# Kernel optimization log

Hardware: AMD Instinct MI355X
Metric: run time of the kernel (lower is better)

## Reference

```python
import jax, jax.numpy as jnp
import numpy as np

TOTAL_LABELS = 81
TOTAL_POS = 128
TOTAL_NEG = 384


def _randomly_select_mask(key, mask, count):
    """Replicates rpn_utils.randomly_select_xyz_mask: keep at most `count`
    randomly-chosen True entries per row (axis=1)."""
    rnd = jax.random.randint(key, mask.shape, 1, count * 10, dtype=jnp.int32)
    scored = mask.astype(jnp.int32) * rnd          # 0 where mask False
    order = jnp.argsort(-scored, axis=1)           # descending sort indices
    rank = jnp.argsort(order, axis=1)              # rank of each position
    return mask & (rank < count)


def setup_inputs() -> dict:
    key = jax.random.key(0)
    k1, k2, k3, k4, k5, k6 = jax.random.split(key, 6)
    B, N, M = 32, 6000, 128
    # Valid normalized boxes (y1,x1,y2,x2): corner + positive extent
    roi_tl = jax.random.uniform(k1, (B, N, 2), minval=0.0, maxval=0.8)
    roi_wh = jax.random.uniform(k2, (B, N, 2), minval=0.01, maxval=0.2)
    roi_bboxes = jnp.concatenate([roi_tl, roi_tl + roi_wh], axis=-1)
    gt_tl = jax.random.uniform(k3, (B, M, 2), minval=0.0, maxval=0.8)
    gt_wh = jax.random.uniform(k4, (B, M, 2), minval=0.05, maxval=0.2)
    gt_boxes = jnp.concatenate([gt_tl, gt_tl + gt_wh], axis=-1)
    gt_labels = jax.random.randint(k5, (B, M), 0, TOTAL_LABELS, dtype=jnp.int32)
    return {"roi_bboxes": roi_bboxes, "gt_boxes": gt_boxes, "gt_labels": gt_labels}


def reference(roi_bboxes, gt_boxes, gt_labels):
    # ---- pairwise IoU (faithful, incl. original gt_area==0 bug) ----
    by1, bx1, by2, bx2 = jnp.split(roi_bboxes, 4, axis=-1)   # each [B,N,1]
    gy1, gx1, gy2, gx2 = jnp.split(gt_boxes, 4, axis=-1)     # each [B,M,1]
    gt_area = jnp.squeeze((gy2 - gy1) * (gx2 - gx2), axis=-1)  # == 0 (original bug)
    bbox_area = jnp.squeeze((by2 - by1) * (bx2 - bx1), axis=-1)
    x_top = jnp.maximum(bx1, jnp.swapaxes(gx1, 1, 2))
    y_top = jnp.maximum(by1, jnp.swapaxes(gy1, 1, 2))
    x_bot = jnp.minimum(bx2, jnp.swapaxes(gx2, 1, 2))
    y_bot = jnp.minimum(by2, jnp.swapaxes(gy2, 1, 2))
    inter = jnp.maximum(x_bot - x_top, 0.0) * jnp.maximum(y_bot - y_top, 0.0)  # [B,N,M]
    union = bbox_area[..., None] + gt_area[:, None, :] - inter
    iou_map = inter / union

    max_idx = jnp.argmax(iou_map, axis=2)   # [B,N]
    merged = jnp.max(iou_map, axis=2)       # [B,N]

    # ---- random positive / negative sampling ----
    skey = jax.random.key(42)
    kp, kn = jax.random.split(skey)
    pos_mask = _randomly_select_mask(kp, merged > 0.5, TOTAL_POS)
    neg_mask = _randomly_select_mask(kn, (merged < 0.5) & (merged > 0.1), TOTAL_NEG)

    # ---- gather matched GT boxes/labels (batch_dims=1 gather) ----
    gt_boxes_map = jax.vmap(lambda g, i: g[i])(gt_boxes, max_idx)     # [B,N,4]
    gt_labels_map = jax.vmap(lambda g, i: g[i])(gt_labels, max_idx)   # [B,N]
    exp_gt = jnp.where(pos_mask[..., None], gt_boxes_map, 0.0)
    pos_lab = jnp.where(pos_mask, gt_labels_map, jnp.int32(-1))
    exp_lab = pos_lab + neg_mask.astype(jnp.int32)  # neg -> 0 (background)

    # ---- bbox delta encoding ----
    bw = roi_bboxes[..., 3] - roi_bboxes[..., 1]
    bh = roi_bboxes[..., 2] - roi_bboxes[..., 0]
    bcx = roi_bboxes[..., 1] + 0.5 * bw
    bcy = roi_bboxes[..., 0] + 0.5 * bh
    gw = exp_gt[..., 3] - exp_gt[..., 1]
    gh = exp_gt[..., 2] - exp_gt[..., 0]
    gcx = exp_gt[..., 1] + 0.5 * gw
    gcy = exp_gt[..., 0] + 0.5 * gh
    bw = jnp.where(bw == 0, 1e-3, bw)
    bh = jnp.where(bh == 0, 1e-3, bh)
    gw_safe = jnp.where(gw == 0, 1.0, gw)  # safe-where: same fwd values, no NaN
    gh_safe = jnp.where(gh == 0, 1.0, gh)
    dx = jnp.where(gw == 0, 0.0, (gcx - bcx) / bw)
    dy = jnp.where(gh == 0, 0.0, (gcy - bcy) / bh)
    dw = jnp.where(gw == 0, 0.0, jnp.log(gw_safe / bw))
    dh = jnp.where(gh == 0, 0.0, jnp.log(gh_safe / bh))
    deltas = jnp.stack([dy, dx, dh, dw], axis=-1)  # [B,N,4]

    # ---- one-hot scatter-multiply ----
    roi_bbox_labels = jax.nn.one_hot(exp_lab, TOTAL_LABELS, dtype=deltas.dtype)  # [B,N,L]; -1 -> all-zero
    roi_bbox_deltas = roi_bbox_labels[..., None] * deltas[:, :, None, :]          # [B,N,L,4]
    return roi_bbox_deltas, roi_bbox_labels
```

## Files before the change

### kernel.cpp

```cpp
#include <hip/hip_runtime.h>
#include <stdint.h>

#define NB 32
#define NN 6000
#define NM 128
#define NL 81
#define NT (NB * NN)
#define SPAN_P 1279u
#define MULT_P 882u
#define SPAN_N 3839u
#define MULT_N 1588u
#define K_POS 128u
#define K_NEG 384u

#define OUT_FLOATS ((size_t)NT * NL * 5)
#define OUT_VEC4 (OUT_FLOATS / 4)

__host__ __device__ __forceinline__ uint32_t rotl32(uint32_t v, uint32_t r) {
  return (v << r) | (v >> (32u - r));
}

__host__ __device__ inline void threefry2x32(uint32_t k0, uint32_t k1,
                                             uint32_t x0, uint32_t x1,
                                             uint32_t& o0, uint32_t& o1) {
  uint32_t kb = k0 ^ k1 ^ 0x1BD11BDAu;
#define TF_ROUND(r) { x0 += x1; x1 = rotl32(x1, r); x1 ^= x0; }
  x0 += k0; x1 += k1;
  TF_ROUND(13u) TF_ROUND(15u) TF_ROUND(26u) TF_ROUND(6u)
  x0 += k1; x1 += kb + 1u;
  TF_ROUND(17u) TF_ROUND(29u) TF_ROUND(16u) TF_ROUND(24u)
  x0 += kb; x1 += k0 + 2u;
  TF_ROUND(13u) TF_ROUND(15u) TF_ROUND(26u) TF_ROUND(6u)
  x0 += k0; x1 += k1 + 3u;
  TF_ROUND(17u) TF_ROUND(29u) TF_ROUND(16u) TF_ROUND(24u)
  x0 += k1; x1 += kb + 4u;
  TF_ROUND(13u) TF_ROUND(15u) TF_ROUND(26u) TF_ROUND(6u)
  x0 += kb; x1 += k0 + 5u;
#undef TF_ROUND
  o0 = x0; o1 = x1;
}

__global__ __launch_bounds__(256) void iou_mask_score(
    const float* __restrict__ roi, const float* __restrict__ gt,
    uint16_t* __restrict__ scp, uint16_t* __restrict__ scn,
    uint8_t* __restrict__ midx, float* __restrict__ out,
    uint32_t k1p0, uint32_t k1p1, uint32_t k2p0, uint32_t k2p1,
    uint32_t k1n0, uint32_t k1n1, uint32_t k2n0, uint32_t k2n1)
{
#pragma clang fp contract(off)
  __shared__ float4 g[NM];
  int b = blockIdx.y;
  if (threadIdx.x < NM)
    g[threadIdx.x] = reinterpret_cast<const float4*>(gt)[b * NM + threadIdx.x];
  __syncthreads();

  {
    float4* o4 = reinterpret_cast<float4*>(out);
    const float4 z = make_float4(0.0f, 0.0f, 0.0f, 0.0f);
    uint32_t gthreads = gridDim.x * gridDim.y * 256u;
    uint32_t i0 = (blockIdx.y * gridDim.x + blockIdx.x) * 256u + threadIdx.x;
    for (uint32_t i = i0; i < (uint32_t)OUT_VEC4; i += gthreads)
      o4[i] = z;
  }

  int n = blockIdx.x * 256 + threadIdx.x;
  if (n >= NN) return;
  size_t t = (size_t)b * NN + n;
  float4 r = reinterpret_cast<const float4*>(roi)[t];
  float by1 = r.x, bx1 = r.y, by2 = r.z, bx2 = r.w;
  float area = (by2 - by1) * (bx2 - bx1);
  float best = -INFINITY; int bi = 0;
  for (int j = 0; j < NM; ++j) {
    float4 q = g[j];
    float xt = fmaxf(bx1, q.y), yt = fmaxf(by1, q.x);
    float xb = fminf(bx2, q.w), yb = fminf(by2, q.z);
    float inter = fmaxf(xb - xt, 0.0f) * fmaxf(yb - yt, 0.0f);
    float uni = area - inter;
    float iou = inter / uni;
    if (iou > best) { best = iou; bi = j; }
  }
  bool pos = best > 0.5f;
  bool neg = (best < 0.5f) && (best > 0.1f);
  uint16_t sp = 0, sn = 0;
  uint32_t a0, a1;
  if (pos) {
    uint32_t h, l;
    threefry2x32(k1p0, k1p1, 0u, (uint32_t)t, a0, a1); h = a0 ^ a1;
    threefry2x32(k2p0, k2p1, 0u, (uint32_t)t, a0, a1); l = a0 ^ a1;
    sp = (uint16_t)(1u + ((h % SPAN_P) * MULT_P + (l % SPAN_P)) % SPAN_P);
  }
  if (neg) {
    uint32_t h, l;
    threefry2x32(k1n0, k1n1, 0u, (uint32_t)t, a0, a1); h = a0 ^ a1;
    threefry2x32(k2n0, k2n1, 0u, (uint32_t)t, a0, a1); l = a0 ^ a1;
    sn = (uint16_t)(1u + ((h % SPAN_N) * MULT_N + (l % SPAN_N)) % SPAN_N);
  }
  scp[t] = sp; scn[t] = sn; midx[t] = (uint8_t)bi;
}

__global__ __launch_bounds__(256) void select_write(
    const uint16_t* __restrict__ scp, const uint16_t* __restrict__ scn,
    const uint8_t* __restrict__ midx,
    const float* __restrict__ roi, const float* __restrict__ gt,
    const int* __restrict__ glab,
    float* __restrict__ out)
{
#pragma clang fp contract(off)
  __shared__ uint32_t hist[3840];
  __shared__ uint32_t csum[256];
  __shared__ uint32_t cpref[256];
  __shared__ int shT;
  __shared__ uint32_t shRem;
  int tid = threadIdx.x;
  int b = blockIdx.x & 31;
  int type = blockIdx.x >> 5;
  const uint16_t* sc = (type ? scn : scp) + (size_t)b * NN;
  const int S = type ? 3840 : 1280;
  const uint32_t K = type ? K_NEG : K_POS;

  for (int s = tid; s < S; s += 256) hist[s] = 0u;
  if (tid == 0) { shT = 0; shRem = 0u; }
  __syncthreads();
  for (int n = tid; n < NN; n += 256) {
    uint32_t s = sc[n];
    if (s) atomicAdd(&hist[s], 1u);
  }
  __syncthreads();
  const int cb = S >> 8;
  int lo = tid * cb, hi = lo + cb;
  uint32_t ms = 0;
  for (int s = lo; s < hi; ++s) ms += hist[s];
  csum[tid] = ms;
  __syncthreads();
  if (tid == 0) {
    uint32_t run = 0;
    for (int c = 255; c >= 0; --c) { cpref[c] = run; run += csum[c]; }
  }
  __syncthreads();
  {
    uint32_t cum = cpref[tid];
    for (int s = hi - 1; s >= lo; --s) {
      uint32_t h = hist[s];
      if (h != 0u && cum < K && cum + h >= K) { shT = s; shRem = K - cum; }
      cum += h;
    }
  }
  __syncthreads();
  const int T = shT;
  const uint32_t rem = shRem;
  const int CH = 24;
  int n0 = tid * CH, n1 = n0 + CH; if (n1 > NN) n1 = NN;
  uint32_t ec = 0;
  if (T > 0) { for (int n = n0; n < n1; ++n) if (sc[n] == (uint16_t)T) ++ec; }
  csum[tid] = ec;
  __syncthreads();
  if (tid == 0) { uint32_t run = 0; for (int c = 0; c < 256; ++c) { cpref[c] = run; run += csum[c]; } }
  __syncthreads();
  uint32_t tr = cpref[tid];
  const size_t labBase = (size_t)NT * NL * 4;
  for (int n = n0; n < n1; ++n) {
    uint32_t s = sc[n];
    if (!s) continue;
    bool keep;
    if ((int)s > T) keep = true;
    else if ((int)s == T) { keep = (tr < rem); ++tr; }
    else keep = false;
    if (!keep) continue;
    size_t t = (size_t)b * NN + n;
    if (type) {
      out[labBase + t * (size_t)NL] = 1.0f;
    } else {
      int mi = midx[t];
      int lab = glab[b * NM + mi];
      float4 r = reinterpret_cast<const float4*>(roi)[t];
      float4 q = reinterpret_cast<const float4*>(gt)[(size_t)b * NM + mi];
      float by1 = r.x, bx1 = r.y, by2 = r.z, bx2 = r.w;
      float gy1 = q.x, gx1 = q.y, gy2 = q.z, gx2 = q.w;
      float bw = bx2 - bx1, bh = by2 - by1;
      float bcx = bx1 + 0.5f * bw, bcy = by1 + 0.5f * bh;
      float gw = gx2 - gx1, gh = gy2 - gy1;
      float gcx = gx1 + 0.5f * gw, gcy = gy1 + 0.5f * gh;
      if (bw == 0.0f) bw = 1e-3f;
      if (bh == 0.0f) bh = 1e-3f;
      float dx = (gw == 0.0f) ? 0.0f : (gcx - bcx) / bw;
      float dy = (gh == 0.0f) ? 0.0f : (gcy - bcy) / bh;
      float dw = (gw == 0.0f) ? 0.0f : logf(gw / bw);
      float dh = (gh == 0.0f) ? 0.0f : logf(gh / bh);
      float4 d; d.x = dy; d.y = dx; d.z = dh; d.w = dw;
      reinterpret_cast<float4*>(out)[t * (size_t)NL + lab] = d;
      out[labBase + t * (size_t)NL + lab] = 1.0f;
    }
  }
}

extern "C" void kernel_launch(void* const* d_in, const int* in_sizes, int n_in,
                              void* d_out, int out_size, void* d_ws, size_t ws_size,
                              hipStream_t stream) {
  (void)in_sizes; (void)n_in; (void)ws_size; (void)out_size;
  const float* roi = (const float*)d_in[0];
  const float* gt  = (const float*)d_in[1];
  const int* glab  = (const int*)d_in[2];
  float* out = (float*)d_out;

  uint16_t* scp = (uint16_t*)d_ws;
  uint16_t* scn = scp + NT;
  uint8_t*  midx = (uint8_t*)(scn + NT);

  uint32_t kp0, kp1, kn0, kn1;
  threefry2x32(0u, 42u, 0u, 0u, kp0, kp1);
  threefry2x32(0u, 42u, 0u, 1u, kn0, kn1);
  uint32_t k1p0, k1p1, k2p0, k2p1, k1n0, k1n1, k2n0, k2n1;
  threefry2x32(kp0, kp1, 0u, 0u, k1p0, k1p1);
  threefry2x32(kp0, kp1, 0u, 1u, k2p0, k2p1);
  threefry2x32(kn0, kn1, 0u, 0u, k1n0, k1n1);
  threefry2x32(kn0, kn1, 0u, 1u, k2n0, k2n1);

  dim3 gridA(24, 32);
  iou_mask_score<<<gridA, 256, 0, stream>>>(roi, gt, scp, scn, midx, out,
      k1p0, k1p1, k2p0, k2p1, k1n0, k1n1, k2n0, k2n1);
  select_write<<<64, 256, 0, stream>>>(scp, scn, midx, roi, gt, glab, out);
}
```

Baseline: 365.8 us.

## Write dense output in one final pass from compact per-ROI label and delta

The output is no longer zeroed and then scatter-patched. The selection kernel now records a compact per-ROI label and delta in workspace, and a new third kernel writes every float4 of the dense one-hot delta and label tensors in one coalesced pass. This removes the zero-fill loop from the IoU kernel and the scattered writes into the large output. The cost is an extra kernel launch, small extra workspace reads, and integer division per output element.

```diff
diff --git a/kernel.cpp b/kernel.cpp
--- a/kernel.cpp
+++ b/kernel.cpp
@@ -13,8 +13,11 @@
 #define K_POS 128u
 #define K_NEG 384u
 
-#define OUT_FLOATS ((size_t)NT * NL * 5)
-#define OUT_VEC4 (OUT_FLOATS / 4)
+#define DELTA_FLOATS ((size_t)NT * NL * 4)
+#define LABEL_FLOATS ((size_t)NT * NL)
+#define DELTA_VEC4 (DELTA_FLOATS / 4)
+#define LABEL_VEC4 (LABEL_FLOATS / 4)
+#define TOTAL_VEC4 (DELTA_VEC4 + LABEL_VEC4)
 
 __host__ __device__ __forceinline__ uint32_t rotl32(uint32_t v, uint32_t r) {
   return (v << r) | (v >> (32u - r));
@@ -43,7 +46,7 @@
 __global__ __launch_bounds__(256) void iou_mask_score(
     const float* __restrict__ roi, const float* __restrict__ gt,
     uint16_t* __restrict__ scp, uint16_t* __restrict__ scn,
-    uint8_t* __restrict__ midx, float* __restrict__ out,
+    uint8_t* __restrict__ midx, int* __restrict__ dlab,
     uint32_t k1p0, uint32_t k1p1, uint32_t k2p0, uint32_t k2p1,
     uint32_t k1n0, uint32_t k1n1, uint32_t k2n0, uint32_t k2n1)
 {
@@ -53,16 +56,6 @@
   if (threadIdx.x < NM)
     g[threadIdx.x] = reinterpret_cast<const float4*>(gt)[b * NM + threadIdx.x];
   __syncthreads();
-
-  {
-    float4* o4 = reinterpret_cast<float4*>(out);
-    const float4 z = make_float4(0.0f, 0.0f, 0.0f, 0.0f);
-    uint32_t gthreads = gridDim.x * gridDim.y * 256u;
-    uint32_t i0 = (blockIdx.y * gridDim.x + blockIdx.x) * 256u + threadIdx.x;
-    for (uint32_t i = i0; i < (uint32_t)OUT_VEC4; i += gthreads)
-      o4[i] = z;
-  }
-
   int n = blockIdx.x * 256 + threadIdx.x;
   if (n >= NN) return;
   size_t t = (size_t)b * NN + n;
@@ -96,14 +89,15 @@
     sn = (uint16_t)(1u + ((h % SPAN_N) * MULT_N + (l % SPAN_N)) % SPAN_N);
   }
   scp[t] = sp; scn[t] = sn; midx[t] = (uint8_t)bi;
-}
-
-__global__ __launch_bounds__(256) void select_write(
+  dlab[t] = -1;
+}
+
+__global__ __launch_bounds__(256) void select_mark(
     const uint16_t* __restrict__ scp, const uint16_t* __restrict__ scn,
     const uint8_t* __restrict__ midx,
     const float* __restrict__ roi, const float* __restrict__ gt,
     const int* __restrict__ glab,
-    float* __restrict__ out)
+    int* __restrict__ dlab, float4* __restrict__ ddelta)
 {
 #pragma clang fp contract(off)
   __shared__ uint32_t hist[3840];
@@ -157,7 +151,6 @@
   if (tid == 0) { uint32_t run = 0; for (int c = 0; c < 256; ++c) { cpref[c] = run; run += csum[c]; } }
   __syncthreads();
   uint32_t tr = cpref[tid];
-  const size_t labBase = (size_t)NT * NL * 4;
   for (int n = n0; n < n1; ++n) {
     uint32_t s = sc[n];
     if (!s) continue;
@@ -168,7 +161,8 @@
     if (!keep) continue;
     size_t t = (size_t)b * NN + n;
     if (type) {
-      out[labBase + t * (size_t)NL] = 1.0f;
+      dlab[t] = 0;
+      ddelta[t] = make_float4(0.0f, 0.0f, 0.0f, 0.0f);
     } else {
       int mi = midx[t];
       int lab = glab[b * NM + mi];
@@ -186,10 +180,48 @@
       float dy = (gh == 0.0f) ? 0.0f : (gcy - bcy) / bh;
       float dw = (gw == 0.0f) ? 0.0f : logf(gw / bw);
       float dh = (gh == 0.0f) ? 0.0f : logf(gh / bh);
-      float4 d; d.x = dy; d.y = dx; d.z = dh; d.w = dw;
-      reinterpret_cast<float4*>(out)[t * (size_t)NL + lab] = d;
-      out[labBase + t * (size_t)NL + lab] = 1.0f;
+      dlab[t] = lab;
+      ddelta[t] = make_float4(dy, dx, dh, dw);
     }
+  }
+}
+
+__global__ __launch_bounds__(256) void write_out(
+    const int* __restrict__ dlab, const float4* __restrict__ ddelta,
+    float4* __restrict__ out4)
+{
+  const float4 z = make_float4(0.0f, 0.0f, 0.0f, 0.0f);
+  uint32_t gsz = gridDim.x * 256u;
+  for (uint32_t i = blockIdx.x * 256u + threadIdx.x; i < (uint32_t)TOTAL_VEC4; i += gsz) {
+    float4 v = z;
+    if (i < (uint32_t)DELTA_VEC4) {
+      uint32_t t = i / (uint32_t)NL;
+      uint32_t s = i - t * (uint32_t)NL;
+      int L = dlab[t];
+      if ((int)s == L) v = ddelta[t];
+    } else {
+      uint32_t f = (i - (uint32_t)DELTA_VEC4) * 4u;
+      uint32_t t = f / (uint32_t)NL;
+      uint32_t s = f - t * (uint32_t)NL;
+      if (s <= (uint32_t)(NL - 4)) {
+        int L = dlab[t];
+        v.x = ((int)s     == L) ? 1.0f : 0.0f;
+        v.y = ((int)s + 1 == L) ? 1.0f : 0.0f;
+        v.z = ((int)s + 2 == L) ? 1.0f : 0.0f;
+        v.w = ((int)s + 3 == L) ? 1.0f : 0.0f;
+      } else {
+        float vv[4];
+#pragma unroll
+        for (int j = 0; j < 4; ++j) {
+          uint32_t fj = f + (uint32_t)j;
+          uint32_t tj = fj / (uint32_t)NL;
+          uint32_t sj = fj - tj * (uint32_t)NL;
+          vv[j] = ((int)sj == dlab[tj]) ? 1.0f : 0.0f;
+        }
+        v.x = vv[0]; v.y = vv[1]; v.z = vv[2]; v.w = vv[3];
+      }
+    }
+    out4[i] = v;
   }
 }
 
@@ -202,7 +234,9 @@
   const int* glab  = (const int*)d_in[2];
   float* out = (float*)d_out;
 
-  uint16_t* scp = (uint16_t*)d_ws;
+  float4* ddelta = (float4*)d_ws;
+  int* dlab = (int*)(ddelta + NT);
+  uint16_t* scp = (uint16_t*)(dlab + NT);
   uint16_t* scn = scp + NT;
   uint8_t*  midx = (uint8_t*)(scn + NT);
 
@@ -216,7 +250,8 @@
   threefry2x32(kn0, kn1, 0u, 1u, k2n0, k2n1);
 
   dim3 gridA(24, 32);
-  iou_mask_score<<<gridA, 256, 0, stream>>>(roi, gt, scp, scn, midx, out,
+  iou_mask_score<<<gridA, 256, 0, stream>>>(roi, gt, scp, scn, midx, dlab,
       k1p0, k1p1, k2p0, k2p1, k1n0, k1n1, k2n0, k2n1);
-  select_write<<<64, 256, 0, stream>>>(scp, scn, midx, roi, gt, glab, out);
-}
+  select_mark<<<64, 256, 0, stream>>>(scp, scn, midx, roi, gt, glab, dlab, ddelta);
+  write_out<<<2048, 256, 0, stream>>>(dlab, ddelta, (float4*)out);
+}
```

Measured after the change: 379.8 us. +3.8%, slower.
